# Optimization experiments

Measured on AMD Instinct MI355X. Metric: run time of the kernel, lower is better.

Reference implementation:

```python
import jax, jax.numpy as jnp
import numpy as np

N = 50000      # nodes
E_RAND = 800000
IN = 256       # in_dim
HID = 64       # num_hidden
H = 4          # heads for GATv2 layers 0,1
C = 32         # num_classes (final layer, 1 head)
SLOPE = 0.2


def setup_inputs() -> dict:
    key = jax.random.key(0)
    ks = jax.random.split(key, 12)
    x = jax.random.normal(ks[0], (N, IN), dtype=jnp.float32)
    src = jax.random.randint(ks[1], (E_RAND,), 0, N, dtype=jnp.int32)
    dst = jax.random.randint(ks[2], (E_RAND,), 0, N, dtype=jnp.int32)
    loops = jnp.arange(N, dtype=jnp.int32)  # self-loops: every node has an in-edge
    src = jnp.concatenate([src, loops])
    dst = jnp.concatenate([dst, loops])
    s = 0.05
    W0 = jax.random.normal(ks[3], (IN, H * HID), dtype=jnp.float32) * s
    a0 = jax.random.normal(ks[4], (H, HID), dtype=jnp.float32) * s
    W1 = jax.random.normal(ks[5], (H * HID, H * HID), dtype=jnp.float32) * s
    a1 = jax.random.normal(ks[6], (H, HID), dtype=jnp.float32) * s
    W2 = jax.random.normal(ks[7], (H * HID, 1 * C), dtype=jnp.float32) * s
    a2 = jax.random.normal(ks[8], (1, C), dtype=jnp.float32) * s
    Wres2 = jax.random.normal(ks[9], (H * HID, C), dtype=jnp.float32) * s
    return {"x": x, "src": src, "dst": dst, "W0": W0, "a0": a0,
            "W1": W1, "a1": a1, "W2": W2, "a2": a2, "Wres2": Wres2}


def _gatv2_layer(h, W, a, src, dst, heads, out, res, activation):
    n = h.shape[0]
    # share_weights=True: same projection for src and dst (DGL GATv2Conv)
    f = (h @ W).reshape(n, heads, out)            # [N,H,D]
    fe = f[src] + f[dst]                          # gather: [E,H,D]
    e = jnp.einsum('ehd,hd->eh', jax.nn.leaky_relu(fe, SLOPE), a)  # [E,H]
    # edge softmax over incoming edges per destination node
    m = jax.ops.segment_max(e, dst, num_segments=n)
    ex = jnp.exp(e - m[dst])
    z = jax.ops.segment_sum(ex, dst, num_segments=n)
    alpha = ex / z[dst]                           # [E,H]
    msg = alpha[:, :, None] * f[src]              # [E,H,D]
    rst = jax.ops.segment_sum(msg, dst, num_segments=n)  # [N,H,D]
    if res is not None:
        rst = rst + res
    if activation:
        rst = jax.nn.elu(rst)
    return rst


def reference(x, src, dst, W0, a0, W1, a1, W2, a2, Wres2):
    # layer 0: no residual, elu, flatten heads
    h = _gatv2_layer(x, W0, a0, src, dst, H, HID, None, True).reshape(N, H * HID)
    # layer 1: residual (in == heads*out -> identity reshape), elu, flatten
    res1 = h.reshape(N, H, HID)
    h = _gatv2_layer(h, W1, a1, src, dst, H, HID, res1, True).reshape(N, H * HID)
    # final layer: residual via res_fc (256 != 1*32), no activation, mean over heads
    res2 = (h @ Wres2).reshape(N, 1, C)
    logits = _gatv2_layer(h, W2, a2, src, dst, 1, C, res2, False).mean(axis=1)
    return logits
```

## Files before the change

### kernel.cpp

```cpp
#include <hip/hip_runtime.h>
#include <hip/hip_bf16.h>

typedef __hip_bfloat16 bf16;
#define SLOPE 0.2f

__device__ __forceinline__ float b2f(bf16 v) { return __bfloat162float(v); }
__device__ __forceinline__ short f2b_raw(float x) {
    bf16 b = __float2bfloat16(x);
    return *reinterpret_cast<short*>(&b);
}

typedef __attribute__((ext_vector_type(8))) short bf16x8;
typedef __attribute__((ext_vector_type(16))) float f32x16;
typedef __attribute__((ext_vector_type(2))) float f32x2;

union Q16 { uint4 q[2]; unsigned u[8]; };

__global__ void k_detect(const void* __restrict__ x, int* __restrict__ flag,
                         int* __restrict__ cnt, int n) {
    int i = blockIdx.x * blockDim.x + threadIdx.x;
    if (i < n) cnt[i] = 0;
    if (blockIdx.x == 0 && threadIdx.x < 64) {
        const unsigned short* u = (const unsigned short*)x;
        int tid = threadIdx.x;
        int nice = 0;
        for (int k = tid; k < 256; k += 64) {
            unsigned int bits = ((unsigned int)u[2 * k]) << 16;
            float v = __uint_as_float(bits);
            float av = fabsf(v);
            if (v == 0.0f || (av > 1e-6f && av < 100.0f)) ++nice;
        }
        for (int off = 32; off > 0; off >>= 1) nice += __shfl_down(nice, off, 64);
        if (tid == 0) *flag = (nice >= 192) ? 0 : 1;
    }
}

__global__ void k_prep(const void* __restrict__ W0, const void* __restrict__ W1,
                       const void* __restrict__ W2, const void* __restrict__ Wr2,
                       const void* __restrict__ a0, const void* __restrict__ a1,
                       const void* __restrict__ a2, bf16* __restrict__ W0p,
                       bf16* __restrict__ W1p, bf16* __restrict__ W2fp,
                       bf16* __restrict__ a0c, bf16* __restrict__ a1c,
                       bf16* __restrict__ a2c, const int* __restrict__ flag) {
    int idx = blockIdx.x * blockDim.x + threadIdx.x;
    int isf = *flag;
    if (idx < 131072) {
        int t = idx & 65535;
        int j = t & 7, L = (t >> 3) & 63, kt = (t >> 9) & 15, nt = t >> 13;
        int n = nt * 32 + (L & 31);
        int k = kt * 16 + (L >> 5) * 8 + j;
        const void* src = (idx < 65536) ? W0 : W1;
        float v = isf ? ((const float*)src)[k * 256 + n] : b2f(((const bf16*)src)[k * 256 + n]);
        bf16* dstp = (idx < 65536) ? W0p : W1p;
        dstp[t] = __float2bfloat16(v);
    } else if (idx < 147456) {
        int t = idx - 131072;
        int j = t & 7, L = (t >> 3) & 63, kt = (t >> 9) & 15, nt = t >> 13;
        int n = nt * 32 + (L & 31);
        int k = kt * 16 + (L >> 5) * 8 + j;
        const void* src = (n < 32) ? W2 : Wr2;
        int nn = n & 31;
        float v = isf ? ((const float*)src)[k * 32 + nn] : b2f(((const bf16*)src)[k * 32 + nn]);
        W2fp[t] = __float2bfloat16(v);
    } else if (idx < 147456 + 256) {
        int t = idx - 147456;
        float v = isf ? ((const float*)a0)[t] : b2f(((const bf16*)a0)[t]);
        a0c[t] = __float2bfloat16(v);
    } else if (idx < 147456 + 512) {
        int t = idx - 147456 - 256;
        float v = isf ? ((const float*)a1)[t] : b2f(((const bf16*)a1)[t]);
        a1c[t] = __float2bfloat16(v);
    } else if (idx < 147456 + 544) {
        int t = idx - 147456 - 512;
        float v = isf ? ((const float*)a2)[t] : b2f(((const bf16*)a2)[t]);
        a2c[t] = __float2bfloat16(v);
    }
}

__global__ void k_hist(const int* __restrict__ dst, int* __restrict__ cnt, int E) {
    int e = blockIdx.x * blockDim.x + threadIdx.x;
    if (e < E) atomicAdd(&cnt[dst[e]], 1);
}

__global__ void k_bsum(const int* __restrict__ cnt, int* __restrict__ bsum, int n) {
    __shared__ int sh[256];
    int base = blockIdx.x * 1024 + threadIdx.x * 4;
    int s = 0;
#pragma unroll
    for (int k = 0; k < 4; ++k) { int i = base + k; if (i < n) s += cnt[i]; }
    sh[threadIdx.x] = s;
    __syncthreads();
    for (int off = 128; off > 0; off >>= 1) {
        if (threadIdx.x < off) sh[threadIdx.x] += sh[threadIdx.x + off];
        __syncthreads();
    }
    if (threadIdx.x == 0) bsum[blockIdx.x] = sh[0];
}

__global__ void k_bscan(int* __restrict__ bsum, int B) {
    __shared__ int sh[1024];
    int t = threadIdx.x;
    int v = (t < B) ? bsum[t] : 0;
    sh[t] = v;
    __syncthreads();
    for (int off = 1; off < 1024; off <<= 1) {
        int u = (t >= off) ? sh[t - off] : 0;
        __syncthreads();
        sh[t] += u;
        __syncthreads();
    }
    if (t < B) bsum[t] = sh[t] - v;
}

__global__ void k_scanwrite(const int* __restrict__ cnt, const int* __restrict__ bsum,
                            int* __restrict__ rowptr, int* __restrict__ cursor, int n, int E) {
    __shared__ int sh[256];
    int base = blockIdx.x * 1024 + threadIdx.x * 4;
    int loc[4];
    int s = 0;
#pragma unroll
    for (int k = 0; k < 4; ++k) {
        int i = base + k;
        loc[k] = (i < n) ? cnt[i] : 0;
        s += loc[k];
    }
    sh[threadIdx.x] = s;
    __syncthreads();
    for (int off = 1; off < 256; off <<= 1) {
        int u = (threadIdx.x >= off) ? sh[threadIdx.x - off] : 0;
        __syncthreads();
        sh[threadIdx.x] += u;
        __syncthreads();
    }
    int run = bsum[blockIdx.x] + sh[threadIdx.x] - s;
#pragma unroll
    for (int k = 0; k < 4; ++k) {
        int i = base + k;
        if (i < n) { rowptr[i] = run; cursor[i] = run; run += loc[k]; }
    }
    if (blockIdx.x == 0 && threadIdx.x == 0) rowptr[n] = E;
}

__global__ void k_scatter(const int* __restrict__ src, const int* __restrict__ dst,
                          int* __restrict__ cursor, int* __restrict__ csr_src, int E) {
    int e = blockIdx.x * blockDim.x + threadIdx.x;
    if (e < E) {
        int p = atomicAdd(&cursor[dst[e]], 1);
        csr_src[p] = src[e];
    }
}

template <int ADAPT>
__global__ void k_gemm_mfma(const void* __restrict__ A, const bf16* __restrict__ Wp,
                            bf16* __restrict__ C, int Nrows, const int* __restrict__ flag) {
    int warp = threadIdx.x >> 6;
    int lane = threadIdx.x & 63;
    int wr = warp >> 1;
    int wc = warp & 1;
    long rowBase = (long)blockIdx.x * 64 + wr * 32;
    int colBase = wc * 128;
    int m = lane & 31;
    int g = lane >> 5;
    long r = rowBase + m;
    if (r >= Nrows) r = Nrows - 1;
    int isf32 = ADAPT ? *flag : 0;
    const short* Ab = (const short*)A + r * 256 + g * 8;
    const float* Af = (const float*)A + r * 256 + g * 8;
    const short* Wps = (const short*)Wp;
    f32x16 acc[4] = {};
    for (int kt = 0; kt < 16; ++kt) {
        bf16x8 af;
        if (ADAPT && isf32) {
            float4 x0 = *(const float4*)(Af + kt * 16);
            float4 x1 = *(const float4*)(Af + kt * 16 + 4);
            union { bf16x8 v; short s[8]; } t;
            t.s[0] = f2b_raw(x0.x); t.s[1] = f2b_raw(x0.y);
            t.s[2] = f2b_raw(x0.z); t.s[3] = f2b_raw(x0.w);
            t.s[4] = f2b_raw(x1.x); t.s[5] = f2b_raw(x1.y);
            t.s[6] = f2b_raw(x1.z); t.s[7] = f2b_raw(x1.w);
            af = t.v;
        } else {
            af = *(const bf16x8*)(Ab + kt * 16);
        }
#pragma unroll
        for (int ct = 0; ct < 4; ++ct) {
            int nt = wc * 4 + ct;
            bf16x8 bfr = *(const bf16x8*)(Wps + (((nt << 4) + kt) << 9) + lane * 8);
            acc[ct] = __builtin_amdgcn_mfma_f32_32x32x16_bf16(af, bfr, acc[ct], 0, 0, 0);
        }
    }
#pragma unroll
    for (int ct = 0; ct < 4; ++ct) {
#pragma unroll
        for (int i = 0; i < 16; ++i) {
            long row = rowBase + (i & 3) + 8 * (i >> 2) + 4 * g;
            if (row < Nrows)
                C[row * 256 + colBase + ct * 32 + m] = __float2bfloat16(acc[ct][i]);
        }
    }
}

__global__ void k_gemm_mfma64(const bf16* __restrict__ A, const bf16* __restrict__ Wp,
                              bf16* __restrict__ C, int Nrows) {
    int warp = threadIdx.x >> 6;
    int lane = threadIdx.x & 63;
    long rowBase = (long)blockIdx.x * 128 + warp * 32;
    int m = lane & 31;
    int g = lane >> 5;
    long r = rowBase + m;
    if (r >= Nrows) r = Nrows - 1;
    const short* Arow = (const short*)A + r * 256 + g * 8;
    const short* Wps = (const short*)Wp;
    f32x16 acc[2] = {};
    for (int kt = 0; kt < 16; ++kt) {
        bf16x8 af = *(const bf16x8*)(Arow + kt * 16);
#pragma unroll
        for (int ct = 0; ct < 2; ++ct) {
            bf16x8 bfr = *(const bf16x8*)(Wps + (((ct << 4) + kt) << 9) + lane * 8);
            acc[ct] = __builtin_amdgcn_mfma_f32_32x32x16_bf16(af, bfr, acc[ct], 0, 0, 0);
        }
    }
#pragma unroll
    for (int ct = 0; ct < 2; ++ct) {
#pragma unroll
        for (int i = 0; i < 16; ++i) {
            long row = rowBase + (i & 3) + 8 * (i >> 2) + 4 * g;
            if (row < Nrows)
                C[row * 64 + ct * 32 + m] = __float2bfloat16(acc[ct][i]);
        }
    }
}

__global__ void k_gat_fused(const uint4* __restrict__ f, const bf16* __restrict__ a,
                            const int* __restrict__ rowptr, const int* __restrict__ csr_src,
                            const uint4* __restrict__ res, uint4* __restrict__ out,
                            int N, int mode) {
    int n = (blockIdx.x * blockDim.x + threadIdx.x) >> 6;
    int lane = threadIdx.x & 63;
    if (n >= N) return;
    int j = lane >> 4, l = lane & 15;

    Q16 fdq, aq;
    fdq.q[0] = f[(long)n * 32 + 2 * l];
    fdq.q[1] = f[(long)n * 32 + 2 * l + 1];
    aq.q[0] = ((const uint4*)a)[2 * l];
    aq.q[1] = ((const uint4*)a)[2 * l + 1];
    f32x2 fd2[8], a6[8], a4[8];
#pragma unroll
    for (int i = 0; i < 8; ++i) {
        f32x2 fv, av;
        fv.x = __uint_as_float(fdq.u[i] << 16);
        fv.y = __uint_as_float(fdq.u[i] & 0xffff0000u);
        av.x = __uint_as_float(aq.u[i] << 16);
        av.y = __uint_as_float(aq.u[i] & 0xffff0000u);
        fd2[i] = fv;
        a6[i] = 0.6f * av;
        a4[i] = 0.4f * av;
    }

    int p0 = rowptr[n], p1 = rowptr[n + 1];
    int iters = (p1 - p0 + 3) >> 2;
    float z = 0.f;
    f32x2 acc[8] = {};

    int p = p0 + j;
    int pc = p1 - 1;
    Q16 A0, A1, B0, B1;
    {
        int s0 = csr_src[min(p, pc)];
        A0.q[0] = f[(long)s0 * 32 + 2 * l];
        A0.q[1] = f[(long)s0 * 32 + 2 * l + 1];
        int s1 = csr_src[min(p + 4, pc)];
        A1.q[0] = f[(long)s1 * 32 + 2 * l];
        A1.q[1] = f[(long)s1 * 32 + 2 * l + 1];
    }
    for (int i = 0; i < iters; i += 2) {
        int s0 = csr_src[min(p + 8, pc)];
        B0.q[0] = f[(long)s0 * 32 + 2 * l];
        B0.q[1] = f[(long)s0 * 32 + 2 * l + 1];
        int s1 = csr_src[min(p + 12, pc)];
        B1.q[0] = f[(long)s1 * 32 + 2 * l];
        B1.q[1] = f[(long)s1 * 32 + 2 * l + 1];

#pragma unroll
        for (int half = 0; half < 2; ++half) {
            if (half == 1 && i + 1 >= iters) break;
            const Q16& cur = half ? A1 : A0;
            int pp = p + half * 4;
            f32x2 fs[8];
            f32x2 t2 = {0.f, 0.f};
#pragma unroll
            for (int k = 0; k < 8; ++k) {
                f32x2 fv;
                fv.x = __uint_as_float(cur.u[k] << 16);
                fv.y = __uint_as_float(cur.u[k] & 0xffff0000u);
                fs[k] = fv;
                f32x2 u = fv + fd2[k];
                f32x2 ua;
                ua.x = __uint_as_float(__float_as_uint(u.x) & 0x7fffffffu);
                ua.y = __uint_as_float(__float_as_uint(u.y) & 0x7fffffffu);
                t2 = a6[k] * u + t2;
                t2 = a4[k] * ua + t2;
            }
            float t = t2.x + t2.y;
            t += __shfl_xor(t, 1);
            t += __shfl_xor(t, 2);
            float wgt = (pp < p1) ? __expf(t) : 0.f;
            z += wgt;
            f32x2 w2 = {wgt, wgt};
#pragma unroll
            for (int k = 0; k < 8; ++k) acc[k] = w2 * fs[k] + acc[k];
        }
        A0 = B0;
        A1 = B1;
        p += 8;
    }
    z += __shfl_xor(z, 16);
    z += __shfl_xor(z, 32);
#pragma unroll
    for (int k = 0; k < 8; ++k) {
        acc[k].x += __shfl_xor(acc[k].x, 16);
        acc[k].x += __shfl_xor(acc[k].x, 32);
        acc[k].y += __shfl_xor(acc[k].y, 16);
        acc[k].y += __shfl_xor(acc[k].y, 32);
    }
    if (j < 2) {
        float invz = 1.f / z;
        float o[8];
#pragma unroll
        for (int k = 0; k < 4; ++k) {
            int kk = j * 4 + k;
            o[2 * k]     = acc[kk].x * invz;
            o[2 * k + 1] = acc[kk].y * invz;
        }
        if (mode == 1) {
            uint4 rq = res[(long)n * 32 + 2 * l + j];
            const unsigned* ru = (const unsigned*)&rq;
#pragma unroll
            for (int k = 0; k < 4; ++k) {
                o[2 * k]     += __uint_as_float(ru[k] << 16);
                o[2 * k + 1] += __uint_as_float(ru[k] & 0xffff0000u);
            }
        }
        union { uint4 q; short s[8]; } ob;
#pragma unroll
        for (int k = 0; k < 8; ++k) {
            float v = o[k] > 0.f ? o[k] : (__expf(o[k]) - 1.f);
            ob.s[k] = f2b_raw(v);
        }
        out[(long)n * 32 + 2 * l + j] = ob.q;
    }
}

__global__ void k_gat_fused_fin(const unsigned* __restrict__ fr2u, const bf16* __restrict__ a2,
                                const int* __restrict__ rowptr, const int* __restrict__ csr_src,
                                void* __restrict__ outraw, int N, const int* __restrict__ flag) {
    int n = (blockIdx.x * blockDim.x + threadIdx.x) >> 6;
    int lane = threadIdx.x & 63;
    if (n >= N) return;
    int j = lane >> 4, l = lane & 15;

    unsigned fdu = fr2u[(long)n * 32 + l];
    unsigned au  = ((const unsigned*)a2)[l];
    f32x2 fd2, a6, a4;
    fd2.x = __uint_as_float(fdu << 16);
    fd2.y = __uint_as_float(fdu & 0xffff0000u);
    float ax = __uint_as_float(au << 16);
    float ay = __uint_as_float(au & 0xffff0000u);
    a6.x = 0.6f * ax; a6.y = 0.6f * ay;
    a4.x = 0.4f * ax; a4.y = 0.4f * ay;

    int p0 = rowptr[n], p1 = rowptr[n + 1];
    int iters = (p1 - p0 + 3) >> 2;
    float z = 0.f;
    f32x2 acc = {0.f, 0.f};

    int p = p0 + j;
    int pc = p1 - 1;
    unsigned A0, A1, B0, B1;
    A0 = fr2u[(long)csr_src[min(p, pc)] * 32 + l];
    A1 = fr2u[(long)csr_src[min(p + 4, pc)] * 32 + l];
    for (int i = 0; i < iters; i += 2) {
        B0 = fr2u[(long)csr_src[min(p + 8, pc)] * 32 + l];
        B1 = fr2u[(long)csr_src[min(p + 12, pc)] * 32 + l];
#pragma unroll
        for (int half = 0; half < 2; ++half) {
            if (half == 1 && i + 1 >= iters) break;
            unsigned cu = half ? A1 : A0;
            int pp = p + half * 4;
            f32x2 fs;
            fs.x = __uint_as_float(cu << 16);
            fs.y = __uint_as_float(cu & 0xffff0000u);
            f32x2 u = fs + fd2;
            f32x2 ua;
            ua.x = __uint_as_float(__float_as_uint(u.x) & 0x7fffffffu);
            ua.y = __uint_as_float(__float_as_uint(u.y) & 0x7fffffffu);
            f32x2 t2 = a6 * u + a4 * ua;
            float t = t2.x + t2.y;
            t += __shfl_xor(t, 1);
            t += __shfl_xor(t, 2);
            t += __shfl_xor(t, 4);
            t += __shfl_xor(t, 8);
            float wgt = (pp < p1) ? __expf(t) : 0.f;
            z += wgt;
            f32x2 w2 = {wgt, wgt};
            acc = w2 * fs + acc;
        }
        A0 = B0;
        A1 = B1;
        p += 8;
    }
    z += __shfl_xor(z, 16);
    z += __shfl_xor(z, 32);
    acc.x += __shfl_xor(acc.x, 16);
    acc.x += __shfl_xor(acc.x, 32);
    acc.y += __shfl_xor(acc.y, 16);
    acc.y += __shfl_xor(acc.y, 32);
    if (j == 0) {
        unsigned ru = fr2u[(long)n * 32 + 16 + l];
        float invz = 1.f / z;
        float o0 = acc.x * invz + __uint_as_float(ru << 16);
        float o1 = acc.y * invz + __uint_as_float(ru & 0xffff0000u);
        if (*flag) {
            float2 ov = {o0, o1};
            ((float2*)outraw)[(long)n * 16 + l] = ov;
        } else {
            unsigned ob = ((unsigned)(unsigned short)f2b_raw(o0)) |
                          (((unsigned)(unsigned short)f2b_raw(o1)) << 16);
            ((unsigned*)outraw)[(long)n * 16 + l] = ob;
        }
    }
}

extern "C" void kernel_launch(void* const* d_in, const int* in_sizes, int n_in,
                              void* d_out, int out_size, void* d_ws, size_t ws_size,
                              hipStream_t stream) {
    const int N = in_sizes[0] / 256;
    const int E = in_sizes[1];

    const void* x   = d_in[0];
    const int*  src = (const int*)d_in[1];
    const int*  dst = (const int*)d_in[2];

    char* w = (char*)d_ws;
    auto alloc = [&](size_t bytes) -> char* {
        char* p = w;
        w += (bytes + 15) & ~(size_t)15;
        return p;
    };
    bf16* buf0 = (bf16*)alloc((size_t)N * 256 * 2);
    bf16* buf1 = (bf16*)alloc((size_t)N * 256 * 2);
    bf16* buf2 = (bf16*)alloc((size_t)N * 256 * 2);
    int* csr_src = (int*)alloc((size_t)E * 4);
    int* rowptr  = (int*)alloc((size_t)(N + 1) * 4);
    int* cursor  = (int*)alloc((size_t)N * 4);
    int* cnt     = (int*)alloc((size_t)N * 4);
    int* bsum    = (int*)alloc((size_t)1024 * 4);
    bf16* W0p  = (bf16*)alloc((size_t)65536 * 2);
    bf16* W1p  = (bf16*)alloc((size_t)65536 * 2);
    bf16* W2fp = (bf16*)alloc((size_t)64 * 256 * 2);
    bf16* a0c  = (bf16*)alloc((size_t)256 * 2);
    bf16* a1c  = (bf16*)alloc((size_t)256 * 2);
    bf16* a2c  = (bf16*)alloc((size_t)32 * 2);
    int*  flag = (int*)alloc(16);

    bf16* hA  = buf1;
    bf16* fB  = buf2;
    bf16* hB  = buf0;
    bf16* fr2 = buf2;

    k_detect<<<(N + 255) / 256, 256, 0, stream>>>(x, flag, cnt, N);
    k_prep<<<(147456 + 544 + 255) / 256, 256, 0, stream>>>(
        d_in[3], d_in[5], d_in[7], d_in[9], d_in[4], d_in[6], d_in[8],
        W0p, W1p, W2fp, a0c, a1c, a2c, flag);

    const int B = (N + 1023) / 1024;
    k_hist<<<(E + 255) / 256, 256, 0, stream>>>(dst, cnt, E);
    k_bsum<<<B, 256, 0, stream>>>(cnt, bsum, N);
    k_bscan<<<1, 1024, 0, stream>>>(bsum, B);
    k_scanwrite<<<B, 256, 0, stream>>>(cnt, bsum, rowptr, cursor, N, E);
    k_scatter<<<(E + 255) / 256, 256, 0, stream>>>(src, dst, cursor, csr_src, E);

    const int ngrid4 = (int)(((long)N * 64 + 255) / 256);

    k_gemm_mfma<1><<<(N + 63) / 64, 256, 0, stream>>>(x, W0p, fB, N, flag);
    k_gat_fused<<<ngrid4, 256, 0, stream>>>((const uint4*)fB, a0c, rowptr, csr_src,
                                            nullptr, (uint4*)hA, N, 0);
    k_gemm_mfma<0><<<(N + 63) / 64, 256, 0, stream>>>(hA, W1p, fB, N, flag);
    k_gat_fused<<<ngrid4, 256, 0, stream>>>((const uint4*)fB, a1c, rowptr, csr_src,
                                            (const uint4*)hA, (uint4*)hB, N, 1);
    k_gemm_mfma64<<<(N + 127) / 128, 256, 0, stream>>>(hB, W2fp, fr2, N);
    k_gat_fused_fin<<<ngrid4, 256, 0, stream>>>((const unsigned*)fr2, a2c, rowptr, csr_src,
                                                d_out, N, flag);
}
```

Before: 442.7 us.

## Merge setup kernels, fuse block scan via last-block ticket, deepen gather prefetch

Folds the dtype-detect and count-zeroing kernel into the weight-prep kernel, and merges the block-sum and block-scan kernels using an atomic ticket so the last block performs the scan. This removes two kernel launches. The GAT aggregation loops now prefetch four edge groups ahead instead of two. The final layer uses 8 lanes per edge with uint2 loads, so each wave processes eight edges at a time. The last-block scan only covers B up to 64 and depends on fence and atomic ordering, and the deeper prefetch raises register pressure.

```diff
diff --git a/kernel.cpp b/kernel.cpp
--- a/kernel.cpp
+++ b/kernel.cpp
@@ -16,11 +16,17 @@
 
 union Q16 { uint4 q[2]; unsigned u[8]; };
 
-__global__ void k_detect(const void* __restrict__ x, int* __restrict__ flag,
-                         int* __restrict__ cnt, int n) {
-    int i = blockIdx.x * blockDim.x + threadIdx.x;
-    if (i < n) cnt[i] = 0;
-    if (blockIdx.x == 0 && threadIdx.x < 64) {
+__global__ void k_prep(const void* __restrict__ x,
+                       const void* __restrict__ W0, const void* __restrict__ W1,
+                       const void* __restrict__ W2, const void* __restrict__ Wr2,
+                       const void* __restrict__ a0, const void* __restrict__ a1,
+                       const void* __restrict__ a2, bf16* __restrict__ W0p,
+                       bf16* __restrict__ W1p, bf16* __restrict__ W2fp,
+                       bf16* __restrict__ a0c, bf16* __restrict__ a1c,
+                       bf16* __restrict__ a2c, int* __restrict__ flag,
+                       int* __restrict__ cnt, int* __restrict__ ticket, int N) {
+    __shared__ int sflag;
+    if (threadIdx.x < 64) {
         const unsigned short* u = (const unsigned short*)x;
         int tid = threadIdx.x;
         int nice = 0;
@@ -31,19 +37,13 @@
             if (v == 0.0f || (av > 1e-6f && av < 100.0f)) ++nice;
         }
         for (int off = 32; off > 0; off >>= 1) nice += __shfl_down(nice, off, 64);
-        if (tid == 0) *flag = (nice >= 192) ? 0 : 1;
-    }
-}
-
-__global__ void k_prep(const void* __restrict__ W0, const void* __restrict__ W1,
-                       const void* __restrict__ W2, const void* __restrict__ Wr2,
-                       const void* __restrict__ a0, const void* __restrict__ a1,
-                       const void* __restrict__ a2, bf16* __restrict__ W0p,
-                       bf16* __restrict__ W1p, bf16* __restrict__ W2fp,
-                       bf16* __restrict__ a0c, bf16* __restrict__ a1c,
-                       bf16* __restrict__ a2c, const int* __restrict__ flag) {
+        if (tid == 0) sflag = (nice >= 192) ? 0 : 1;
+    }
+    __syncthreads();
+    int isf = sflag;
     int idx = blockIdx.x * blockDim.x + threadIdx.x;
-    int isf = *flag;
+    if (blockIdx.x == 0 && threadIdx.x == 0) { *flag = isf; *ticket = 0; }
+    if (idx < N) cnt[idx] = 0;
     if (idx < 131072) {
         int t = idx & 65535;
         int j = t & 7, L = (t >> 3) & 63, kt = (t >> 9) & 15, nt = t >> 13;
@@ -82,8 +82,10 @@
     if (e < E) atomicAdd(&cnt[dst[e]], 1);
 }
 
-__global__ void k_bsum(const int* __restrict__ cnt, int* __restrict__ bsum, int n) {
+__global__ void k_bsum_scan(const int* __restrict__ cnt, int* __restrict__ bsum,
+                            int* __restrict__ ticket, int n, int B) {
     __shared__ int sh[256];
+    __shared__ int lastFlag;
     int base = blockIdx.x * 1024 + threadIdx.x * 4;
     int s = 0;
 #pragma unroll
@@ -94,22 +96,24 @@
         if (threadIdx.x < off) sh[threadIdx.x] += sh[threadIdx.x + off];
         __syncthreads();
     }
-    if (threadIdx.x == 0) bsum[blockIdx.x] = sh[0];
-}
-
-__global__ void k_bscan(int* __restrict__ bsum, int B) {
-    __shared__ int sh[1024];
-    int t = threadIdx.x;
-    int v = (t < B) ? bsum[t] : 0;
-    sh[t] = v;
+    if (threadIdx.x == 0) {
+        atomicExch(&bsum[blockIdx.x], sh[0]);
+        __threadfence();
+        int t = atomicAdd(ticket, 1);
+        lastFlag = (t == B - 1) ? 1 : 0;
+    }
     __syncthreads();
-    for (int off = 1; off < 1024; off <<= 1) {
-        int u = (t >= off) ? sh[t - off] : 0;
-        __syncthreads();
-        sh[t] += u;
-        __syncthreads();
-    }
-    if (t < B) bsum[t] = sh[t] - v;
+    if (lastFlag && threadIdx.x < 64) {
+        int tid = threadIdx.x;
+        int v = (tid < B) ? atomicAdd(&bsum[tid], 0) : 0;
+        int xv = v;
+#pragma unroll
+        for (int off = 1; off < 64; off <<= 1) {
+            int y = __shfl_up(xv, off, 64);
+            if (tid >= off) xv += y;
+        }
+        if (tid < B) bsum[tid] = xv - v;
+    }
 }
 
 __global__ void k_scanwrite(const int* __restrict__ cnt, const int* __restrict__ bsum,
@@ -260,60 +264,56 @@
 
     int p0 = rowptr[n], p1 = rowptr[n + 1];
     int iters = (p1 - p0 + 3) >> 2;
+    int pc = p1 - 1;
     float z = 0.f;
     f32x2 acc[8] = {};
 
+    Q16 A0, A1, B0, B1;
+    auto loadQ = [&](Q16& Q, int pp) {
+        int s = csr_src[min(pp, pc)];
+        const uint4* fp = f + ((long)s << 5) + 2 * l;
+        Q.q[0] = fp[0];
+        Q.q[1] = fp[1];
+    };
+    auto proc = [&](const Q16& cur, int pp) {
+        f32x2 fs[8];
+        f32x2 t2 = {0.f, 0.f};
+#pragma unroll
+        for (int k = 0; k < 8; ++k) {
+            f32x2 fv;
+            fv.x = __uint_as_float(cur.u[k] << 16);
+            fv.y = __uint_as_float(cur.u[k] & 0xffff0000u);
+            fs[k] = fv;
+            f32x2 u = fv + fd2[k];
+            f32x2 ua;
+            ua.x = __uint_as_float(__float_as_uint(u.x) & 0x7fffffffu);
+            ua.y = __uint_as_float(__float_as_uint(u.y) & 0x7fffffffu);
+            t2 = a6[k] * u + t2;
+            t2 = a4[k] * ua + t2;
+        }
+        float t = t2.x + t2.y;
+        t += __shfl_xor(t, 1);
+        t += __shfl_xor(t, 2);
+        float wgt = (pp < p1) ? __expf(t) : 0.f;
+        z += wgt;
+        f32x2 w2 = {wgt, wgt};
+#pragma unroll
+        for (int k = 0; k < 8; ++k) acc[k] = w2 * fs[k] + acc[k];
+    };
+
     int p = p0 + j;
-    int pc = p1 - 1;
-    Q16 A0, A1, B0, B1;
-    {
-        int s0 = csr_src[min(p, pc)];
-        A0.q[0] = f[(long)s0 * 32 + 2 * l];
-        A0.q[1] = f[(long)s0 * 32 + 2 * l + 1];
-        int s1 = csr_src[min(p + 4, pc)];
-        A1.q[0] = f[(long)s1 * 32 + 2 * l];
-        A1.q[1] = f[(long)s1 * 32 + 2 * l + 1];
-    }
-    for (int i = 0; i < iters; i += 2) {
-        int s0 = csr_src[min(p + 8, pc)];
-        B0.q[0] = f[(long)s0 * 32 + 2 * l];
-        B0.q[1] = f[(long)s0 * 32 + 2 * l + 1];
-        int s1 = csr_src[min(p + 12, pc)];
-        B1.q[0] = f[(long)s1 * 32 + 2 * l];
-        B1.q[1] = f[(long)s1 * 32 + 2 * l + 1];
-
-#pragma unroll
-        for (int half = 0; half < 2; ++half) {
-            if (half == 1 && i + 1 >= iters) break;
-            const Q16& cur = half ? A1 : A0;
-            int pp = p + half * 4;
-            f32x2 fs[8];
-            f32x2 t2 = {0.f, 0.f};
-#pragma unroll
-            for (int k = 0; k < 8; ++k) {
-                f32x2 fv;
-                fv.x = __uint_as_float(cur.u[k] << 16);
-                fv.y = __uint_as_float(cur.u[k] & 0xffff0000u);
-                fs[k] = fv;
-                f32x2 u = fv + fd2[k];
-                f32x2 ua;
-                ua.x = __uint_as_float(__float_as_uint(u.x) & 0x7fffffffu);
-                ua.y = __uint_as_float(__float_as_uint(u.y) & 0x7fffffffu);
-                t2 = a6[k] * u + t2;
-                t2 = a4[k] * ua + t2;
-            }
-            float t = t2.x + t2.y;
-            t += __shfl_xor(t, 1);
-            t += __shfl_xor(t, 2);
-            float wgt = (pp < p1) ? __expf(t) : 0.f;
-            z += wgt;
-            f32x2 w2 = {wgt, wgt};
-#pragma unroll
-            for (int k = 0; k < 8; ++k) acc[k] = w2 * fs[k] + acc[k];
-        }
-        A0 = B0;
-        A1 = B1;
-        p += 8;
+    loadQ(A0, p);
+    loadQ(A1, p + 4);
+    for (int i = 0; i < iters; i += 4) {
+        loadQ(B0, p + 8);
+        loadQ(B1, p + 12);
+        proc(A0, p);
+        if (i + 1 < iters) proc(A1, p + 4);
+        loadQ(A0, p + 16);
+        loadQ(A1, p + 20);
+        if (i + 2 < iters) proc(B0, p + 8);
+        if (i + 3 < iters) proc(B1, p + 12);
+        p += 16;
     }
     z += __shfl_xor(z, 16);
     z += __shfl_xor(z, 32);
@@ -352,82 +352,110 @@
     }
 }
 
-__global__ void k_gat_fused_fin(const unsigned* __restrict__ fr2u, const bf16* __restrict__ a2,
+__global__ void k_gat_fused_fin(const uint2* __restrict__ fr2u2, const bf16* __restrict__ a2,
                                 const int* __restrict__ rowptr, const int* __restrict__ csr_src,
                                 void* __restrict__ outraw, int N, const int* __restrict__ flag) {
     int n = (blockIdx.x * blockDim.x + threadIdx.x) >> 6;
     int lane = threadIdx.x & 63;
     if (n >= N) return;
-    int j = lane >> 4, l = lane & 15;
-
-    unsigned fdu = fr2u[(long)n * 32 + l];
-    unsigned au  = ((const unsigned*)a2)[l];
-    f32x2 fd2, a6, a4;
-    fd2.x = __uint_as_float(fdu << 16);
-    fd2.y = __uint_as_float(fdu & 0xffff0000u);
-    float ax = __uint_as_float(au << 16);
-    float ay = __uint_as_float(au & 0xffff0000u);
-    a6.x = 0.6f * ax; a6.y = 0.6f * ay;
-    a4.x = 0.4f * ax; a4.y = 0.4f * ay;
+    int j = lane >> 3, l = lane & 7;
+
+    uint2 fdu = fr2u2[((long)n << 4) + l];
+    uint2 au  = ((const uint2*)a2)[l];
+    f32x2 fd0, fd1, a60, a61, a40, a41;
+    fd0.x = __uint_as_float(fdu.x << 16);
+    fd0.y = __uint_as_float(fdu.x & 0xffff0000u);
+    fd1.x = __uint_as_float(fdu.y << 16);
+    fd1.y = __uint_as_float(fdu.y & 0xffff0000u);
+    {
+        f32x2 av0, av1;
+        av0.x = __uint_as_float(au.x << 16);
+        av0.y = __uint_as_float(au.x & 0xffff0000u);
+        av1.x = __uint_as_float(au.y << 16);
+        av1.y = __uint_as_float(au.y & 0xffff0000u);
+        a60 = 0.6f * av0; a61 = 0.6f * av1;
+        a40 = 0.4f * av0; a41 = 0.4f * av1;
+    }
 
     int p0 = rowptr[n], p1 = rowptr[n + 1];
-    int iters = (p1 - p0 + 3) >> 2;
+    int iters = (p1 - p0 + 7) >> 3;
+    int pc = p1 - 1;
     float z = 0.f;
-    f32x2 acc = {0.f, 0.f};
+    f32x2 acc0 = {0.f, 0.f}, acc1 = {0.f, 0.f};
+
+    uint2 A0, A1, B0, B1;
+    auto loadU = [&](uint2& Q, int pp) {
+        int s = csr_src[min(pp, pc)];
+        Q = fr2u2[((long)s << 4) + l];
+    };
+    auto proc = [&](uint2 cu, int pp) {
+        f32x2 fs0, fs1;
+        fs0.x = __uint_as_float(cu.x << 16);
+        fs0.y = __uint_as_float(cu.x & 0xffff0000u);
+        fs1.x = __uint_as_float(cu.y << 16);
+        fs1.y = __uint_as_float(cu.y & 0xffff0000u);
+        f32x2 u0 = fs0 + fd0, u1 = fs1 + fd1;
+        f32x2 ua0, ua1;
+        ua0.x = __uint_as_float(__float_as_uint(u0.x) & 0x7fffffffu);
+        ua0.y = __uint_as_float(__float_as_uint(u0.y) & 0x7fffffffu);
+        ua1.x = __uint_as_float(__float_as_uint(u1.x) & 0x7fffffffu);
+        ua1.y = __uint_as_float(__float_as_uint(u1.y) & 0x7fffffffu);
+        f32x2 t2 = a60 * u0;
+        t2 = a40 * ua0 + t2;
+        t2 = a61 * u1 + t2;
+        t2 = a41 * ua1 + t2;
+        float t = t2.x + t2.y;
+        t += __shfl_xor(t, 1);
+        t += __shfl_xor(t, 2);
+        t += __shfl_xor(t, 4);
+        float wgt = (pp < p1) ? __expf(t) : 0.f;
+        z += wgt;
+        f32x2 w2 = {wgt, wgt};
+        acc0 = w2 * fs0 + acc0;
+        acc1 = w2 * fs1 + acc1;
+    };
 
     int p = p0 + j;
-    int pc = p1 - 1;
-    unsigned A0, A1, B0, B1;
-    A0 = fr2u[(long)csr_src[min(p, pc)] * 32 + l];
-    A1 = fr2u[(long)csr_src[min(p + 4, pc)] * 32 + l];
-    for (int i = 0; i < iters; i += 2) {
-        B0 = fr2u[(long)csr_src[min(p + 8, pc)] * 32 + l];
-        B1 = fr2u[(long)csr_src[min(p + 12, pc)] * 32 + l];
-#pragma unroll
-        for (int half = 0; half < 2; ++half) {
-            if (half == 1 && i + 1 >= iters) break;
-            unsigned cu = half ? A1 : A0;
-            int pp = p + half * 4;
-            f32x2 fs;
-            fs.x = __uint_as_float(cu << 16);
-            fs.y = __uint_as_float(cu & 0xffff0000u);
-            f32x2 u = fs + fd2;
-            f32x2 ua;
-            ua.x = __uint_as_float(__float_as_uint(u.x) & 0x7fffffffu);
-            ua.y = __uint_as_float(__float_as_uint(u.y) & 0x7fffffffu);
-            f32x2 t2 = a6 * u + a4 * ua;
-            float t = t2.x + t2.y;
-            t += __shfl_xor(t, 1);
-            t += __shfl_xor(t, 2);
-            t += __shfl_xor(t, 4);
-            t += __shfl_xor(t, 8);
-            float wgt = (pp < p1) ? __expf(t) : 0.f;
-            z += wgt;
-            f32x2 w2 = {wgt, wgt};
-            acc = w2 * fs + acc;
-        }
-        A0 = B0;
-        A1 = B1;
-        p += 8;
-    }
+    loadU(A0, p);
+    loadU(A1, p + 8);
+    for (int i = 0; i < iters; i += 4) {
+        loadU(B0, p + 16);
+        loadU(B1, p + 24);
+        proc(A0, p);
+        if (i + 1 < iters) proc(A1, p + 8);
+        loadU(A0, p + 32);
+        loadU(A1, p + 40);
+        if (i + 2 < iters) proc(B0, p + 16);
+        if (i + 3 < iters) proc(B1, p + 24);
+        p += 32;
+    }
+    z += __shfl_xor(z, 8);
     z += __shfl_xor(z, 16);
     z += __shfl_xor(z, 32);
-    acc.x += __shfl_xor(acc.x, 16);
-    acc.x += __shfl_xor(acc.x, 32);
-    acc.y += __shfl_xor(acc.y, 16);
-    acc.y += __shfl_xor(acc.y, 32);
+#pragma unroll
+    for (int s = 8; s <= 32; s <<= 1) {
+        acc0.x += __shfl_xor(acc0.x, s);
+        acc0.y += __shfl_xor(acc0.y, s);
+        acc1.x += __shfl_xor(acc1.x, s);
+        acc1.y += __shfl_xor(acc1.y, s);
+    }
     if (j == 0) {
-        unsigned ru = fr2u[(long)n * 32 + 16 + l];
+        uint2 ru = fr2u2[((long)n << 4) + 8 + l];
         float invz = 1.f / z;
-        float o0 = acc.x * invz + __uint_as_float(ru << 16);
-        float o1 = acc.y * invz + __uint_as_float(ru & 0xffff0000u);
+        float o0 = acc0.x * invz + __uint_as_float(ru.x << 16);
+        float o1 = acc0.y * invz + __uint_as_float(ru.x & 0xffff0000u);
+        float o2 = acc1.x * invz + __uint_as_float(ru.y << 16);
+        float o3 = acc1.y * invz + __uint_as_float(ru.y & 0xffff0000u);
         if (*flag) {
-            float2 ov = {o0, o1};
-            ((float2*)outraw)[(long)n * 16 + l] = ov;
+            float4 ov = {o0, o1, o2, o3};
+            ((float4*)outraw)[(long)n * 8 + l] = ov;
         } else {
-            unsigned ob = ((unsigned)(unsigned short)f2b_raw(o0)) |
-                          (((unsigned)(unsigned short)f2b_raw(o1)) << 16);
-            ((unsigned*)outraw)[(long)n * 16 + l] = ob;
+            uint2 ob;
+            ob.x = ((unsigned)(unsigned short)f2b_raw(o0)) |
+                   (((unsigned)(unsigned short)f2b_raw(o1)) << 16);
+            ob.y = ((unsigned)(unsigned short)f2b_raw(o2)) |
+                   (((unsigned)(unsigned short)f2b_raw(o3)) << 16);
+            ((uint2*)outraw)[(long)n * 8 + l] = ob;
         }
     }
 }
@@ -463,21 +491,22 @@
     bf16* a1c  = (bf16*)alloc((size_t)256 * 2);
     bf16* a2c  = (bf16*)alloc((size_t)32 * 2);
     int*  flag = (int*)alloc(16);
+    int*  ticket = (int*)alloc(16);
 
     bf16* hA  = buf1;
     bf16* fB  = buf2;
     bf16* hB  = buf0;
     bf16* fr2 = buf2;
 
-    k_detect<<<(N + 255) / 256, 256, 0, stream>>>(x, flag, cnt, N);
-    k_prep<<<(147456 + 544 + 255) / 256, 256, 0, stream>>>(
-        d_in[3], d_in[5], d_in[7], d_in[9], d_in[4], d_in[6], d_in[8],
-        W0p, W1p, W2fp, a0c, a1c, a2c, flag);
+    int prepN = 147456 + 544;
+    if (prepN < N) prepN = N;
+    k_prep<<<(prepN + 255) / 256, 256, 0, stream>>>(
+        x, d_in[3], d_in[5], d_in[7], d_in[9], d_in[4], d_in[6], d_in[8],
+        W0p, W1p, W2fp, a0c, a1c, a2c, flag, cnt, ticket, N);
 
     const int B = (N + 1023) / 1024;
     k_hist<<<(E + 255) / 256, 256, 0, stream>>>(dst, cnt, E);
-    k_bsum<<<B, 256, 0, stream>>>(cnt, bsum, N);
-    k_bscan<<<1, 1024, 0, stream>>>(bsum, B);
+    k_bsum_scan<<<B, 256, 0, stream>>>(cnt, bsum, ticket, N, B);
     k_scanwrite<<<B, 256, 0, stream>>>(cnt, bsum, rowptr, cursor, N, E);
     k_scatter<<<(E + 255) / 256, 256, 0, stream>>>(src, dst, cursor, csr_src, E);
 
@@ -490,6 +519,6 @@
     k_gat_fused<<<ngrid4, 256, 0, stream>>>((const uint4*)fB, a1c, rowptr, csr_src,
                                             (const uint4*)hA, (uint4*)hB, N, 1);
     k_gemm_mfma64<<<(N + 127) / 128, 256, 0, stream>>>(hB, W2fp, fr2, N);
-    k_gat_fused_fin<<<ngrid4, 256, 0, stream>>>((const unsigned*)fr2, a2c, rowptr, csr_src,
+    k_gat_fused_fin<<<ngrid4, 256, 0, stream>>>((const uint2*)fr2, a2c, rowptr, csr_src,
                                                 d_out, N, flag);
 }
```

After: 562.1 us. 1.27x slower.
